# Optimization experiments

Measured on AMD Instinct MI355X. Metric: run time of the kernel, lower is better.

## Reference

```python
import jax, jax.numpy as jnp
import numpy as np

C = 512
K = 3
DIL1 = 1  # dilation[0]
EPS = 1e-9


def _get_padding(kernel_size, dilation=1):
    return (kernel_size * dilation - dilation) // 2


def _upsample2_linear(x):
    # F.interpolate(x, scale_factor=2, mode='linear', align_corners=False)
    # x: [B, C, T] -> [B, C, 2T]
    T = x.shape[-1]
    coord = (jnp.arange(2 * T, dtype=x.dtype) + 0.5) * 0.5 - 0.5
    coord = jnp.maximum(coord, 0.0)  # PyTorch clamps source coord at 0
    i0 = jnp.floor(coord).astype(jnp.int32)
    i1 = jnp.minimum(i0 + 1, T - 1)
    w1 = coord - i0.astype(x.dtype)
    w0 = 1.0 - w1
    return x[..., i0] * w0 + x[..., i1] * w1


def _downsample2_avg(x):
    # AvgPool1d(kernel_size=2, stride=2)
    B, Ch, T = x.shape
    return x.reshape(B, Ch, T // 2, 2).mean(axis=-1)


def _snakebeta_act1d(x, alpha, beta):
    a = jnp.exp(alpha)[None, :, None]
    b = jnp.exp(beta)[None, :, None]
    up = _upsample2_linear(x)
    y = up + (1.0 - jnp.cos(2.0 * a * up)) / (2.0 * b + EPS)
    return _downsample2_avg(y)


def _wn_weight(v, g):
    # weight_norm: w = g * v / ||v||, norm over (in, k) dims per out channel
    norm = jnp.sqrt(jnp.sum(v * v, axis=(1, 2), keepdims=True))
    return g[:, None, None] * v / norm


def _conv1d(x, w, bias, dilation, pad):
    y = jax.lax.conv_general_dilated(
        x, w, window_strides=(1,), padding=[(pad, pad)],
        rhs_dilation=(dilation,), dimension_numbers=('NCH', 'OIH', 'NCH'))
    return y + bias[None, :, None]


def setup_inputs() -> dict:
    key = jax.random.key(0)
    ks = jax.random.split(key, 11)
    B, T = 8, 8192
    x = jax.random.normal(ks[0], (B, C, T), dtype=jnp.float32)
    v1 = jax.random.normal(ks[1], (C, C, K), dtype=jnp.float32) * 0.05
    g1 = jnp.ones((C,), dtype=jnp.float32)
    bias1 = jax.random.normal(ks[2], (C,), dtype=jnp.float32) * 0.01
    v2 = jax.random.normal(ks[3], (C, C, K), dtype=jnp.float32) * 0.05
    g2 = jnp.ones((C,), dtype=jnp.float32)
    bias2 = jax.random.normal(ks[4], (C,), dtype=jnp.float32) * 0.01
    # SnakeBeta logscale params (init 0 in torch; small random for testing)
    alpha1 = jax.random.normal(ks[5], (C,), dtype=jnp.float32) * 0.1
    beta1 = jax.random.normal(ks[6], (C,), dtype=jnp.float32) * 0.1
    alpha2 = jax.random.normal(ks[7], (C,), dtype=jnp.float32) * 0.1
    beta2 = jax.random.normal(ks[8], (C,), dtype=jnp.float32) * 0.1
    return {"x": x, "v1": v1, "g1": g1, "bias1": bias1,
            "v2": v2, "g2": g2, "bias2": bias2,
            "alpha1": alpha1, "beta1": beta1, "alpha2": alpha2, "beta2": beta2}


def reference(x, v1, g1, bias1, v2, g2, bias2, alpha1, beta1, alpha2, beta2):
    pad1 = _get_padding(K, DIL1)
    pad2 = _get_padding(K, 1)
    xt = _snakebeta_act1d(x, alpha1, beta1)
    xt = _conv1d(xt, _wn_weight(v1, g1), bias1, DIL1, pad1)
    xt = _snakebeta_act1d(xt, alpha2, beta2)
    xt = _conv1d(xt, _wn_weight(v2, g2), bias2, 1, pad2)
    return xt + x[:, :, :xt.shape[2]]
```

## Files before the change

kernel.cpp:

```cpp
#include <hip/hip_runtime.h>

typedef unsigned short ushort_t;
typedef __bf16 bf16x8 __attribute__((ext_vector_type(8)));
typedef float f32x4 __attribute__((ext_vector_type(4)));

#define B_  8
#define C_  512
#define T_  8192
#define TP_ 8194

static __device__ __forceinline__ float bf2f(ushort_t u) {
    return __uint_as_float(((unsigned)u) << 16);
}
static __device__ __forceinline__ ushort_t f2bf(float f) {
    unsigned u = __float_as_uint(f);
    unsigned r = (u + 0x7FFFu + ((u >> 16) & 1u)) >> 16;
    return (ushort_t)r;
}

static __device__ __forceinline__ void gl_lds16(const void* g, void* l) {
    __builtin_amdgcn_global_load_lds(
        (const __attribute__((address_space(1))) void*)g,
        (__attribute__((address_space(3))) void*)l, 16, 0, 0);
}

template <int BF> struct In;
template <> struct In<0> {
    static __device__ __forceinline__ float ld(const void* p, size_t i) {
        return ((const float*)p)[i];
    }
};
template <> struct In<1> {
    static __device__ __forceinline__ float ld(const void* p, size_t i) {
        return bf2f(((const ushort_t*)p)[i]);
    }
};

#define P_G1 0
#define P_B1 512
#define P_G2 1024
#define P_B2 1536
#define P_A1 2048
#define P_I1 2560
#define P_A2 3072
#define P_I2 3584

__global__ void param_kernel(const void* g1, const void* bias1, const void* g2, const void* bias2,
                             const void* alpha1, const void* beta1, const void* alpha2, const void* beta2,
                             float* __restrict__ pr, int* __restrict__ flag) {
    int i = threadIdx.x;
    unsigned guard = ((const unsigned*)g1)[0];
    int bf = (guard == 0x3F803F80u) ? 1 : 0;
    if (i == 0) *flag = bf;
    float g1v, b1v, g2v, b2v, a1v, be1v, a2v, be2v;
    if (bf) {
        g1v = In<1>::ld(g1, i);  b1v = In<1>::ld(bias1, i);
        g2v = In<1>::ld(g2, i);  b2v = In<1>::ld(bias2, i);
        a1v = In<1>::ld(alpha1, i); be1v = In<1>::ld(beta1, i);
        a2v = In<1>::ld(alpha2, i); be2v = In<1>::ld(beta2, i);
    } else {
        g1v = In<0>::ld(g1, i);  b1v = In<0>::ld(bias1, i);
        g2v = In<0>::ld(g2, i);  b2v = In<0>::ld(bias2, i);
        a1v = In<0>::ld(alpha1, i); be1v = In<0>::ld(beta1, i);
        a2v = In<0>::ld(alpha2, i); be2v = In<0>::ld(beta2, i);
    }
    pr[P_G1 + i] = g1v;
    pr[P_B1 + i] = b1v;
    pr[P_G2 + i] = g2v;
    pr[P_B2 + i] = b2v;
    pr[P_A1 + i] = __expf(a1v);
    pr[P_I1 + i] = 1.0f / (2.0f * __expf(be1v) + 1e-9f);
    pr[P_A2 + i] = __expf(a2v);
    pr[P_I2 + i] = 1.0f / (2.0f * __expf(be2v) + 1e-9f);
}

template <int BF>
__global__ void wn_kernel(const void* __restrict__ v1, const void* __restrict__ v2,
                          const float* __restrict__ pr, const int* __restrict__ flag,
                          ushort_t* __restrict__ W1, ushort_t* __restrict__ W2) {
    if (*flag != BF) return;
    const void* v = blockIdx.y ? v2 : v1;
    float g = pr[(blockIdx.y ? P_G2 : P_G1) + blockIdx.x];
    ushort_t* W = blockIdx.y ? W2 : W1;
    int co = blockIdx.x;
    int tid = threadIdx.x;
    size_t base = (size_t)co * 1536;
    float vals[6];
    float sum = 0.f;
    #pragma unroll
    for (int i = 0; i < 6; ++i) {
        float f = In<BF>::ld(v, base + tid + i * 256);
        vals[i] = f;
        sum += f * f;
    }
    #pragma unroll
    for (int o = 32; o > 0; o >>= 1) sum += __shfl_down(sum, o, 64);
    __shared__ float red[4];
    if ((tid & 63) == 0) red[tid >> 6] = sum;
    __syncthreads();
    float tot = red[0] + red[1] + red[2] + red[3];
    float scale = g / sqrtf(tot);
    #pragma unroll
    for (int i = 0; i < 6; ++i) {
        int j = tid + i * 256;
        int cin = j / 3, k = j - cin * 3;
        W[(k * C_ + co) * C_ + cin] = f2bf(vals[i] * scale);
    }
}

__global__ void zero_pad_kernel(ushort_t* __restrict__ h) {
    int i = blockIdx.x * 256 + threadIdx.x;
    int b = i >> 10;
    int r = (i >> 9) & 1;
    int c = i & 511;
    h[((size_t)b * TP_ + (r ? (TP_ - 1) : 0)) * C_ + c] = 0;
}

template <int BF>
__global__ void act1_kernel(const void* __restrict__ x,
                            const float* __restrict__ pr, const int* __restrict__ flag,
                            ushort_t* __restrict__ h) {
    if (*flag != BF) return;
    __shared__ float s[64][65];
    int c0 = blockIdx.x * 64, t0 = blockIdx.y * 64, b = blockIdx.z;
    int tid = threadIdx.x;
    int cl = tid >> 2, seg = tid & 3;
    int c = c0 + cl;
    float a = pr[P_A1 + c];
    float inv2b = pr[P_I1 + c];
    size_t xbase = ((size_t)b * C_ + c) << 13;
    int tbase = t0 + seg * 16;
    float xv[18];
    if (BF) {
        const ushort_t* xp = (const ushort_t*)x + xbase;
        #pragma unroll
        for (int q = 0; q < 2; ++q) {
            uint4 v = *(const uint4*)(xp + tbase + q * 8);
            const ushort_t* pv = (const ushort_t*)&v;
            #pragma unroll
            for (int j = 0; j < 8; ++j) xv[1 + q * 8 + j] = bf2f(pv[j]);
        }
        xv[0]  = bf2f(xp[max(tbase - 1, 0)]);
        xv[17] = bf2f(xp[min(tbase + 16, T_ - 1)]);
    } else {
        const float* xp = (const float*)x + xbase;
        #pragma unroll
        for (int q = 0; q < 4; ++q) {
            float4 v = *(const float4*)(xp + tbase + q * 4);
            xv[1 + q * 4 + 0] = v.x;
            xv[1 + q * 4 + 1] = v.y;
            xv[1 + q * 4 + 2] = v.z;
            xv[1 + q * 4 + 3] = v.w;
        }
        xv[0]  = xp[max(tbase - 1, 0)];
        xv[17] = xp[min(tbase + 16, T_ - 1)];
    }
    #pragma unroll
    for (int j = 0; j < 16; ++j) {
        float xm = xv[j], xc = xv[j + 1], xp2 = xv[j + 2];
        float u0 = 0.25f * xm + 0.75f * xc;
        float u1 = 0.75f * xc + 0.25f * xp2;
        float s0 = u0 + (1.0f - __cosf(2.0f * a * u0)) * inv2b;
        float s1 = u1 + (1.0f - __cosf(2.0f * a * u1)) * inv2b;
        s[cl][seg * 16 + j] = 0.5f * (s0 + s1);
    }
    __syncthreads();
    int tl = tid >> 2;
    int t = t0 + tl;
    ushort_t* hrow = h + ((size_t)b * TP_ + (t + 1)) * C_ + c0 + seg * 16;
    #pragma unroll
    for (int q = 0; q < 4; ++q) {
        int cb = seg * 16 + q * 4;
        ushort4 w;
        w.x = f2bf(s[cb + 0][tl]);
        w.y = f2bf(s[cb + 1][tl]);
        w.z = f2bf(s[cb + 2][tl]);
        w.w = f2bf(s[cb + 3][tl]);
        *(ushort4*)(hrow + q * 4) = w;
    }
}

__global__ void act2_kernel(const ushort_t* __restrict__ z,
                            const float* __restrict__ pr,
                            ushort_t* __restrict__ h) {
    size_t idx = (size_t)blockIdx.x * 256 + threadIdx.x;
    int c = idx & (C_ - 1);
    int t = (idx >> 9) & (T_ - 1);
    int b = (int)(idx >> 22);
    const ushort_t* zb = z + ((size_t)b << 22);
    float zc = bf2f(zb[((size_t)t << 9) + c]);
    float zm = bf2f(zb[((size_t)max(t - 1, 0) << 9) + c]);
    float zp = bf2f(zb[((size_t)min(t + 1, T_ - 1) << 9) + c]);
    float a = pr[P_A2 + c];
    float inv2b = pr[P_I2 + c];
    float u0 = 0.25f * zm + 0.75f * zc;
    float u1 = 0.75f * zc + 0.25f * zp;
    float s0 = u0 + (1.0f - __cosf(2.0f * a * u0)) * inv2b;
    float s1 = u1 + (1.0f - __cosf(2.0f * a * u1)) * inv2b;
    h[((size_t)b * TP_ + t + 1) * C_ + c] = f2bf(0.5f * (s0 + s1));
}

struct ConvAcc {
    f32x4 acc[4][4];
    int m0, t0, b, l15, qd, wm, wn;
};

static __device__ __forceinline__ void conv_main(const ushort_t* __restrict__ Xt,
                                                 const ushort_t* __restrict__ W,
                                                 ConvAcc& S) {
    __shared__ __align__(16) ushort_t sA[3 * 128 * 32];
    __shared__ __align__(16) ushort_t sB[130 * 32];

    int tid = threadIdx.x;
    int lane = tid & 63, wid = tid >> 6;
    int wbase = tid & ~63;
    S.m0 = blockIdx.x * 128;
    S.t0 = blockIdx.y * 128;
    S.b  = blockIdx.z;
    S.wm = (wid >> 1) * 64;
    S.wn = (wid & 1) * 64;
    S.l15 = lane & 15;
    S.qd  = lane >> 4;
    #pragma unroll
    for (int mi = 0; mi < 4; ++mi)
        #pragma unroll
        for (int ni = 0; ni < 4; ++ni)
            S.acc[mi][ni] = (f32x4){0.f, 0.f, 0.f, 0.f};

    const ushort_t* xb = Xt + ((size_t)S.b * TP_ + S.t0) * C_;

    for (int ck = 0; ck < 16; ++ck) {
        int cin0 = ck * 32;
        #pragma unroll
        for (int i = 0; i < 6; ++i) {
            int idx = tid + i * 256;
            int tap = idx >> 9;
            int rem = idx & 511;
            int row = rem >> 2, part = rem & 3;
            const ushort_t* gp = W + (((size_t)((tap << 9) + S.m0 + row)) << 9) + cin0 + (part << 3);
            gl_lds16(gp, sA + (size_t)(i * 256 + wbase) * 8);
        }
        #pragma unroll
        for (int i = 0; i < 2; ++i) {
            int idx = tid + i * 256;
            int row = idx >> 2, part = idx & 3;
            const ushort_t* gp = xb + (size_t)row * C_ + cin0 + (part << 3);
            gl_lds16(gp, sB + (size_t)(i * 256 + wbase) * 8);
        }
        if (tid < 8) {
            int row = 128 + (tid >> 2), part = tid & 3;
            const uint4* gp = (const uint4*)(xb + (size_t)row * C_ + cin0 + (part << 3));
            *(uint4*)(sB + row * 32 + (part << 3)) = *gp;
        }
        __syncthreads();
        #pragma unroll
        for (int tap = 0; tap < 3; ++tap) {
            bf16x8 af[4], bfr[4];
            #pragma unroll
            for (int mi = 0; mi < 4; ++mi)
                af[mi] = *(const bf16x8*)(sA + tap * 4096 + (S.wm + mi * 16 + S.l15) * 32 + (S.qd << 3));
            #pragma unroll
            for (int ni = 0; ni < 4; ++ni)
                bfr[ni] = *(const bf16x8*)(sB + (S.wn + ni * 16 + S.l15 + tap) * 32 + (S.qd << 3));
            #pragma unroll
            for (int mi = 0; mi < 4; ++mi)
                #pragma unroll
                for (int ni = 0; ni < 4; ++ni)
                    S.acc[mi][ni] = __builtin_amdgcn_mfma_f32_16x16x32_bf16(af[mi], bfr[ni], S.acc[mi][ni], 0, 0, 0);
        }
        __syncthreads();
    }
}

__global__ __launch_bounds__(256) void conv1_kernel(const ushort_t* __restrict__ Xt,
                                                    const ushort_t* __restrict__ W,
                                                    const float* __restrict__ pr,
                                                    ushort_t* __restrict__ out) {
    ConvAcc S;
    conv_main(Xt, W, S);
    ushort_t* ob = out + ((size_t)S.b << 22);
    #pragma unroll
    for (int mi = 0; mi < 4; ++mi) {
        int cb = S.m0 + S.wm + mi * 16 + S.qd * 4;
        float b0 = pr[P_B1 + cb], b1 = pr[P_B1 + cb + 1];
        float b2 = pr[P_B1 + cb + 2], b3 = pr[P_B1 + cb + 3];
        #pragma unroll
        for (int ni = 0; ni < 4; ++ni) {
            int t = S.t0 + S.wn + ni * 16 + S.l15;
            ushort4 w;
            w.x = f2bf(S.acc[mi][ni][0] + b0);
            w.y = f2bf(S.acc[mi][ni][1] + b1);
            w.z = f2bf(S.acc[mi][ni][2] + b2);
            w.w = f2bf(S.acc[mi][ni][3] + b3);
            *(ushort4*)(ob + ((size_t)t << 9) + cb) = w;
        }
    }
}

template <int BF>
__global__ __launch_bounds__(256) void conv2_kernel(const ushort_t* __restrict__ Xt,
                                                    const ushort_t* __restrict__ W,
                                                    const float* __restrict__ pr,
                                                    const int* __restrict__ flag,
                                                    const void* __restrict__ xres,
                                                    void* __restrict__ out) {
    if (*flag != BF) return;
    ConvAcc S;
    conv_main(Xt, W, S);
    #pragma unroll
    for (int mi = 0; mi < 4; ++mi) {
        int cb = S.m0 + S.wm + mi * 16 + S.qd * 4;
        #pragma unroll
        for (int i = 0; i < 4; ++i) {
            float bi = pr[P_B2 + cb + i];
            size_t rowbase = ((size_t)S.b * C_ + cb + i) << 13;
            #pragma unroll
            for (int ni = 0; ni < 4; ++ni) {
                int t = S.t0 + S.wn + ni * 16 + S.l15;
                float val = S.acc[mi][ni][i] + bi + In<BF>::ld(xres, rowbase + t);
                if (BF) ((ushort_t*)out)[rowbase + t] = f2bf(val);
                else    ((float*)out)[rowbase + t] = val;
            }
        }
    }
}

extern "C" void kernel_launch(void* const* d_in, const int* in_sizes, int n_in,
                              void* d_out, int out_size, void* d_ws, size_t ws_size,
                              hipStream_t stream) {
    const void* x      = d_in[0];
    const void* v1     = d_in[1];
    const void* g1     = d_in[2];
    const void* bias1  = d_in[3];
    const void* v2     = d_in[4];
    const void* g2     = d_in[5];
    const void* bias2  = d_in[6];
    const void* alpha1 = d_in[7];
    const void* beta1  = d_in[8];
    const void* alpha2 = d_in[9];
    const void* beta2  = d_in[10];

    char* ws = (char*)d_ws;
    const size_t H_BYTES = (size_t)B_ * TP_ * C_ * 2;
    ushort_t* h_buf = (ushort_t*)ws;
    ushort_t* W1n   = (ushort_t*)(ws + H_BYTES);
    ushort_t* W2n   = W1n + 3 * C_ * C_;
    float*    pr    = (float*)(W2n + 3 * C_ * C_);
    int*      flag  = (int*)(pr + 8 * 512);
    ushort_t* z1 = (ushort_t*)d_out;

    param_kernel<<<1, 512, 0, stream>>>(g1, bias1, g2, bias2, alpha1, beta1, alpha2, beta2, pr, flag);
    wn_kernel<0><<<dim3(C_, 2), 256, 0, stream>>>(v1, v2, pr, flag, W1n, W2n);
    wn_kernel<1><<<dim3(C_, 2), 256, 0, stream>>>(v1, v2, pr, flag, W1n, W2n);
    zero_pad_kernel<<<32, 256, 0, stream>>>(h_buf);
    act1_kernel<0><<<dim3(C_ / 64, T_ / 64, B_), 256, 0, stream>>>(x, pr, flag, h_buf);
    act1_kernel<1><<<dim3(C_ / 64, T_ / 64, B_), 256, 0, stream>>>(x, pr, flag, h_buf);
    conv1_kernel<<<dim3(C_ / 128, T_ / 128, B_), 256, 0, stream>>>(h_buf, W1n, pr, z1);
    act2_kernel<<<(unsigned)((size_t)B_ * T_ * C_ / 256), 256, 0, stream>>>(z1, pr, h_buf);
    conv2_kernel<0><<<dim3(C_ / 128, T_ / 128, B_), 256, 0, stream>>>(h_buf, W2n, pr, flag, x, d_out);
    conv2_kernel<1><<<dim3(C_ / 128, T_ / 128, B_), 256, 0, stream>>>(h_buf, W2n, pr, flag, x, d_out);
}
```

Measured before the change: 559.6 us.

## Merge dtype-templated kernels, vectorize act2, prefetch conv halo row

```diff
diff --git a/kernel.cpp b/kernel.cpp
--- a/kernel.cpp
+++ b/kernel.cpp
@@ -74,11 +74,10 @@
     pr[P_I2 + i] = 1.0f / (2.0f * __expf(be2v) + 1e-9f);
 }
 
-template <int BF>
 __global__ void wn_kernel(const void* __restrict__ v1, const void* __restrict__ v2,
                           const float* __restrict__ pr, const int* __restrict__ flag,
                           ushort_t* __restrict__ W1, ushort_t* __restrict__ W2) {
-    if (*flag != BF) return;
+    int bf = *flag;
     const void* v = blockIdx.y ? v2 : v1;
     float g = pr[(blockIdx.y ? P_G2 : P_G1) + blockIdx.x];
     ushort_t* W = blockIdx.y ? W2 : W1;
@@ -87,11 +86,20 @@
     size_t base = (size_t)co * 1536;
     float vals[6];
     float sum = 0.f;
-    #pragma unroll
-    for (int i = 0; i < 6; ++i) {
-        float f = In<BF>::ld(v, base + tid + i * 256);
-        vals[i] = f;
-        sum += f * f;
+    if (bf) {
+        #pragma unroll
+        for (int i = 0; i < 6; ++i) {
+            float f = In<1>::ld(v, base + tid + i * 256);
+            vals[i] = f;
+            sum += f * f;
+        }
+    } else {
+        #pragma unroll
+        for (int i = 0; i < 6; ++i) {
+            float f = In<0>::ld(v, base + tid + i * 256);
+            vals[i] = f;
+            sum += f * f;
+        }
     }
     #pragma unroll
     for (int o = 32; o > 0; o >>= 1) sum += __shfl_down(sum, o, 64);
@@ -116,12 +124,11 @@
     h[((size_t)b * TP_ + (r ? (TP_ - 1) : 0)) * C_ + c] = 0;
 }
 
-template <int BF>
 __global__ void act1_kernel(const void* __restrict__ x,
                             const float* __restrict__ pr, const int* __restrict__ flag,
                             ushort_t* __restrict__ h) {
-    if (*flag != BF) return;
     __shared__ float s[64][65];
+    int bf = *flag;
     int c0 = blockIdx.x * 64, t0 = blockIdx.y * 64, b = blockIdx.z;
     int tid = threadIdx.x;
     int cl = tid >> 2, seg = tid & 3;
@@ -131,7 +138,7 @@
     size_t xbase = ((size_t)b * C_ + c) << 13;
     int tbase = t0 + seg * 16;
     float xv[18];
-    if (BF) {
+    if (bf) {
         const ushort_t* xp = (const ushort_t*)x + xbase;
         #pragma unroll
         for (int q = 0; q < 2; ++q) {
@@ -183,21 +190,38 @@
 __global__ void act2_kernel(const ushort_t* __restrict__ z,
                             const float* __restrict__ pr,
                             ushort_t* __restrict__ h) {
-    size_t idx = (size_t)blockIdx.x * 256 + threadIdx.x;
-    int c = idx & (C_ - 1);
-    int t = (idx >> 9) & (T_ - 1);
-    int b = (int)(idx >> 22);
-    const ushort_t* zb = z + ((size_t)b << 22);
-    float zc = bf2f(zb[((size_t)t << 9) + c]);
-    float zm = bf2f(zb[((size_t)max(t - 1, 0) << 9) + c]);
-    float zp = bf2f(zb[((size_t)min(t + 1, T_ - 1) << 9) + c]);
-    float a = pr[P_A2 + c];
-    float inv2b = pr[P_I2 + c];
-    float u0 = 0.25f * zm + 0.75f * zc;
-    float u1 = 0.75f * zc + 0.25f * zp;
-    float s0 = u0 + (1.0f - __cosf(2.0f * a * u0)) * inv2b;
-    float s1 = u1 + (1.0f - __cosf(2.0f * a * u1)) * inv2b;
-    h[((size_t)b * TP_ + t + 1) * C_ + c] = f2bf(0.5f * (s0 + s1));
+    const int NV = B_ * T_ * (C_ / 8);
+    int stride = gridDim.x * blockDim.x;
+    for (int v = blockIdx.x * blockDim.x + threadIdx.x; v < NV; v += stride) {
+        int c8 = v & 63;
+        int t  = (v >> 6) & (T_ - 1);
+        int b  = v >> 19;
+        int c0 = c8 << 3;
+        const ushort_t* zb = z + ((size_t)b << 22);
+        uint4 vc = *(const uint4*)(zb + ((size_t)t << 9) + c0);
+        uint4 vm = *(const uint4*)(zb + ((size_t)max(t - 1, 0) << 9) + c0);
+        uint4 vp = *(const uint4*)(zb + ((size_t)min(t + 1, T_ - 1) << 9) + c0);
+        float4 a0 = *(const float4*)(pr + P_A2 + c0);
+        float4 a1 = *(const float4*)(pr + P_A2 + c0 + 4);
+        float4 i0 = *(const float4*)(pr + P_I2 + c0);
+        float4 i1 = *(const float4*)(pr + P_I2 + c0 + 4);
+        float av[8] = {a0.x, a0.y, a0.z, a0.w, a1.x, a1.y, a1.z, a1.w};
+        float iv[8] = {i0.x, i0.y, i0.z, i0.w, i1.x, i1.y, i1.z, i1.w};
+        const ushort_t* pc = (const ushort_t*)&vc;
+        const ushort_t* pm = (const ushort_t*)&vm;
+        const ushort_t* pp = (const ushort_t*)&vp;
+        ushort_t ov[8];
+        #pragma unroll
+        for (int j = 0; j < 8; ++j) {
+            float zc = bf2f(pc[j]), zm = bf2f(pm[j]), zp = bf2f(pp[j]);
+            float u0 = 0.25f * zm + 0.75f * zc;
+            float u1 = 0.75f * zc + 0.25f * zp;
+            float s0 = u0 + (1.0f - __cosf(2.0f * av[j] * u0)) * iv[j];
+            float s1 = u1 + (1.0f - __cosf(2.0f * av[j] * u1)) * iv[j];
+            ov[j] = f2bf(0.5f * (s0 + s1));
+        }
+        *(uint4*)(h + ((size_t)b * TP_ + t + 1) * C_ + c0) = *(const uint4*)ov;
+    }
 }
 
 struct ConvAcc {
@@ -229,6 +253,11 @@
 
     const ushort_t* xb = Xt + ((size_t)S.b * TP_ + S.t0) * C_;
 
+    int hrow = 128 + (tid >> 2), hpart = tid & 3;
+    const ushort_t* hbase = xb + (size_t)hrow * C_ + (hpart << 3);
+    uint4 hv;
+    if (tid < 8) hv = *(const uint4*)hbase;
+
     for (int ck = 0; ck < 16; ++ck) {
         int cin0 = ck * 32;
         #pragma unroll
@@ -248,9 +277,8 @@
             gl_lds16(gp, sB + (size_t)(i * 256 + wbase) * 8);
         }
         if (tid < 8) {
-            int row = 128 + (tid >> 2), part = tid & 3;
-            const uint4* gp = (const uint4*)(xb + (size_t)row * C_ + cin0 + (part << 3));
-            *(uint4*)(sB + row * 32 + (part << 3)) = *gp;
+            *(uint4*)(sB + hrow * 32 + (hpart << 3)) = hv;
+            if (ck < 15) hv = *(const uint4*)(hbase + cin0 + 32);
         }
         __syncthreads();
         #pragma unroll
@@ -297,29 +325,45 @@
     }
 }
 
-template <int BF>
 __global__ __launch_bounds__(256) void conv2_kernel(const ushort_t* __restrict__ Xt,
                                                     const ushort_t* __restrict__ W,
                                                     const float* __restrict__ pr,
                                                     const int* __restrict__ flag,
                                                     const void* __restrict__ xres,
                                                     void* __restrict__ out) {
-    if (*flag != BF) return;
+    int bf = *flag;
     ConvAcc S;
     conv_main(Xt, W, S);
-    #pragma unroll
-    for (int mi = 0; mi < 4; ++mi) {
-        int cb = S.m0 + S.wm + mi * 16 + S.qd * 4;
-        #pragma unroll
-        for (int i = 0; i < 4; ++i) {
-            float bi = pr[P_B2 + cb + i];
-            size_t rowbase = ((size_t)S.b * C_ + cb + i) << 13;
-            #pragma unroll
-            for (int ni = 0; ni < 4; ++ni) {
-                int t = S.t0 + S.wn + ni * 16 + S.l15;
-                float val = S.acc[mi][ni][i] + bi + In<BF>::ld(xres, rowbase + t);
-                if (BF) ((ushort_t*)out)[rowbase + t] = f2bf(val);
-                else    ((float*)out)[rowbase + t] = val;
+    if (bf) {
+        #pragma unroll
+        for (int mi = 0; mi < 4; ++mi) {
+            int cb = S.m0 + S.wm + mi * 16 + S.qd * 4;
+            #pragma unroll
+            for (int i = 0; i < 4; ++i) {
+                float bi = pr[P_B2 + cb + i];
+                size_t rowbase = ((size_t)S.b * C_ + cb + i) << 13;
+                #pragma unroll
+                for (int ni = 0; ni < 4; ++ni) {
+                    int t = S.t0 + S.wn + ni * 16 + S.l15;
+                    float val = S.acc[mi][ni][i] + bi + bf2f(((const ushort_t*)xres)[rowbase + t]);
+                    ((ushort_t*)out)[rowbase + t] = f2bf(val);
+                }
+            }
+        }
+    } else {
+        #pragma unroll
+        for (int mi = 0; mi < 4; ++mi) {
+            int cb = S.m0 + S.wm + mi * 16 + S.qd * 4;
+            #pragma unroll
+            for (int i = 0; i < 4; ++i) {
+                float bi = pr[P_B2 + cb + i];
+                size_t rowbase = ((size_t)S.b * C_ + cb + i) << 13;
+                #pragma unroll
+                for (int ni = 0; ni < 4; ++ni) {
+                    int t = S.t0 + S.wn + ni * 16 + S.l15;
+                    float val = S.acc[mi][ni][i] + bi + ((const float*)xres)[rowbase + t];
+                    ((float*)out)[rowbase + t] = val;
+                }
             }
         }
     }
@@ -350,13 +394,10 @@
     ushort_t* z1 = (ushort_t*)d_out;
 
     param_kernel<<<1, 512, 0, stream>>>(g1, bias1, g2, bias2, alpha1, beta1, alpha2, beta2, pr, flag);
-    wn_kernel<0><<<dim3(C_, 2), 256, 0, stream>>>(v1, v2, pr, flag, W1n, W2n);
-    wn_kernel<1><<<dim3(C_, 2), 256, 0, stream>>>(v1, v2, pr, flag, W1n, W2n);
+    wn_kernel<<<dim3(C_, 2), 256, 0, stream>>>(v1, v2, pr, flag, W1n, W2n);
     zero_pad_kernel<<<32, 256, 0, stream>>>(h_buf);
-    act1_kernel<0><<<dim3(C_ / 64, T_ / 64, B_), 256, 0, stream>>>(x, pr, flag, h_buf);
-    act1_kernel<1><<<dim3(C_ / 64, T_ / 64, B_), 256, 0, stream>>>(x, pr, flag, h_buf);
+    act1_kernel<<<dim3(C_ / 64, T_ / 64, B_), 256, 0, stream>>>(x, pr, flag, h_buf);
     conv1_kernel<<<dim3(C_ / 128, T_ / 128, B_), 256, 0, stream>>>(h_buf, W1n, pr, z1);
-    act2_kernel<<<(unsigned)((size_t)B_ * T_ * C_ / 256), 256, 0, stream>>>(z1, pr, h_buf);
-    conv2_kernel<0><<<dim3(C_ / 128, T_ / 128, B_), 256, 0, stream>>>(h_buf, W2n, pr, flag, x, d_out);
-    conv2_kernel<1><<<dim3(C_ / 128, T_ / 128, B_), 256, 0, stream>>>(h_buf, W2n, pr, flag, x, d_out);
-}
+    act2_kernel<<<2048, 256, 0, stream>>>(z1, pr, h_buf);
+    conv2_kernel<<<dim3(C_ / 128, T_ / 128, B_), 256, 0, stream>>>(h_buf, W2n, pr, flag, x, d_out);
+}
```

Result: faster. 543.3 us (-2.9%).
